# Kernel tuning notes

Measured on AMD Instinct MI355X. Metric: run time of the kernel, lower is better.

## Reference

```python
import jax, jax.numpy as jnp
import numpy as np

N, E, DIM, H, EDIM = 50000, 800000, 128, 4, 16
C = DIM // H  # per-head channels = 32

def _ln(x, g, b, eps=1e-5):
    mu = jnp.mean(x, -1, keepdims=True)
    var = jnp.mean((x - mu) ** 2, -1, keepdims=True)
    return (x - mu) * jax.lax.rsqrt(var + eps) * g + b

def setup_inputs() -> dict:
    key = jax.random.key(0)
    ks = jax.random.split(key, 16)
    s = lambda d: 1.0 / np.sqrt(d)
    inp = {
        'x': jax.random.normal(ks[0], (N, DIM), jnp.float32),
        'edge_index_s': jax.random.randint(ks[1], (2, E), 0, N, jnp.int64),
        'edge_attr_s': jax.random.normal(ks[2], (E, EDIM), jnp.float32),
        'Wq': jax.random.normal(ks[3], (DIM, DIM), jnp.float32) * s(DIM),
        'bq': jnp.zeros((DIM,), jnp.float32),
        'Wk': jax.random.normal(ks[4], (DIM, DIM), jnp.float32) * s(DIM),
        'bk': jnp.zeros((DIM,), jnp.float32),
        'Wv': jax.random.normal(ks[5], (DIM, DIM), jnp.float32) * s(DIM),
        'bv': jnp.zeros((DIM,), jnp.float32),
        'We': jax.random.normal(ks[6], (EDIM, DIM), jnp.float32) * s(EDIM),
        'be': jnp.zeros((DIM,), jnp.float32),
        'Ws': jax.random.normal(ks[7], (DIM, DIM), jnp.float32) * s(DIM),
        'bs': jnp.zeros((DIM,), jnp.float32),
        'Wbeta': jax.random.normal(ks[8], (3 * DIM, 1), jnp.float32) * s(3 * DIM),
        'g1': jnp.ones((DIM,), jnp.float32),
        'b1': jnp.zeros((DIM,), jnp.float32),
        'Wf1': jax.random.normal(ks[9], (DIM, 4 * DIM), jnp.float32) * s(DIM),
        'bf1': jnp.zeros((4 * DIM,), jnp.float32),
        'Wf2': jax.random.normal(ks[10], (4 * DIM, DIM), jnp.float32) * s(4 * DIM),
        'bf2': jnp.zeros((DIM,), jnp.float32),
        'g2': jnp.ones((DIM,), jnp.float32),
        'b2': jnp.zeros((DIM,), jnp.float32),
    }
    return inp

def reference(x, edge_index_s, edge_attr_s, Wq, bq, Wk, bk, Wv, bv, We, be,
              Ws, bs, Wbeta, g1, b1, Wf1, bf1, Wf2, bf2, g2, b2):
    src, dst = edge_index_s[0], edge_index_s[1]
    # project + reshape to [N, H, C]
    q = (x @ Wq + bq).reshape(N, H, C)
    k = (x @ Wk + bk).reshape(N, H, C)
    v = (x @ Wv + bv).reshape(N, H, C)
    e = (edge_attr_s @ We + be).reshape(E, H, C)
    # gather along edges (irregular access)
    kj = k[src] + e  # [E, H, C]
    vj = v[src] + e
    alpha = jnp.einsum('ehc,ehc->eh', q[dst], kj) / jnp.sqrt(jnp.float32(C))
    # segment softmax over incoming edges of each dst node
    m = jax.ops.segment_max(alpha, dst, num_segments=N)  # [N, H]
    a = jnp.exp(alpha - m[dst])
    denom = jax.ops.segment_sum(a, dst, num_segments=N)
    a = a / (denom[dst] + 1e-16)
    out = jax.ops.segment_sum(a[:, :, None] * vj, dst, num_segments=N)  # [N, H, C]
    out = out.reshape(N, DIM)
    # beta-gated skip (TransformerConv beta=True)
    xr = x @ Ws + bs
    beta = jax.nn.sigmoid(jnp.concatenate([out, xr, out - xr], -1) @ Wbeta)  # [N, 1]
    xs = beta * xr + (1.0 - beta) * out
    # residual + LN + FFN + LN
    h = _ln(x + xs, g1, b1)
    ff = jax.nn.relu(h @ Wf1 + bf1) @ Wf2 + bf2
    return _ln(h + ff, g2, b2)
```

## Files before the change

kernel.cpp:

```cpp
#include <hip/hip_runtime.h>
#include <hip/hip_bf16.h>

#define NN 50000
#define EE 800000
#define DIMM 128

typedef __attribute__((ext_vector_type(8))) short bf16x8;
typedef __attribute__((ext_vector_type(8))) unsigned short us8;
typedef __attribute__((ext_vector_type(4))) float f32x4;

static __device__ __forceinline__ unsigned short f2bf(float f) {
    unsigned int u = __float_as_uint(f);
    unsigned int r = (u + 0x7fffu + ((u >> 16) & 1u)) >> 16;
    return (unsigned short)r;
}
static __device__ __forceinline__ float bf2f(unsigned short s) {
    return __uint_as_float(((unsigned int)s) << 16);
}

__global__ __launch_bounds__(256) void pack_w(
    const float* __restrict__ Wq, const float* __restrict__ Wk,
    const float* __restrict__ Wv, const float* __restrict__ Ws,
    const float* __restrict__ bq, const float* __restrict__ bk,
    const float* __restrict__ bv, const float* __restrict__ bs,
    const float* __restrict__ Wf1, const float* __restrict__ Wf2,
    unsigned short* __restrict__ wqkvsT, unsigned short* __restrict__ wf1T,
    unsigned short* __restrict__ wf2T, float* __restrict__ biasq)
{
    int i = blockIdx.x * 256 + threadIdx.x;
    if (i < 65536) {
        int n = i >> 7, k = i & 127;
        int sel = n >> 7, col = n & 127;
        const float* W = sel == 0 ? Wq : sel == 1 ? Wk : sel == 2 ? Wv : Ws;
        wqkvsT[i] = f2bf(W[k * 128 + col]);
    } else if (i < 131072) {
        int j = i - 65536; int n = j >> 7, k = j & 127;
        wf1T[j] = f2bf(Wf1[k * 512 + n]);
    } else if (i < 196608) {
        int j = i - 131072; int n = j >> 9, k = j & 511;
        wf2T[j] = f2bf(Wf2[k * 128 + n]);
    } else if (i < 197120) {
        int j = i - 196608; int sel = j >> 7;
        const float* bp = sel == 0 ? bq : sel == 1 ? bk : sel == 2 ? bv : bs;
        biasq[j] = bp[j & 127];
    }
}

template<bool A_BF16, int EPI>
__global__ __launch_bounds__(256) void gemm_k(
    const void* __restrict__ Ap, const unsigned short* __restrict__ Bt,
    const float* __restrict__ bias, void* __restrict__ Cp,
    float* __restrict__ qb, unsigned short* __restrict__ kvb, float* __restrict__ xrb,
    int M, int Nn, int K)
{
    __shared__ unsigned short As[128][72];
    __shared__ unsigned short Bs[128][72];
    int tid = threadIdx.x;
    int nb = Nn >> 7;
    int bm = blockIdx.x / nb, bn = blockIdx.x % nb;
    int w = tid >> 6, lane = tid & 63;
    int wm = w >> 1, wn = w & 1;
    int lr = lane & 15, quad = lane >> 4;

    f32x4 acc[4][4];
    #pragma unroll
    for (int i = 0; i < 4; i++)
        #pragma unroll
        for (int j = 0; j < 4; j++) { f32x4 z = {0.f, 0.f, 0.f, 0.f}; acc[i][j] = z; }

    for (int kc = 0; kc < K; kc += 64) {
        #pragma unroll
        for (int it = 0; it < 4; ++it) {
            int row = it * 32 + (tid >> 3);
            int k8 = (tid & 7) * 8;
            int rg = bm * 128 + row;
            us8 st = {0, 0, 0, 0, 0, 0, 0, 0};
            if (rg < M) {
                if constexpr (A_BF16) {
                    st = *(const us8*)((const unsigned short*)Ap + (size_t)rg * K + kc + k8);
                } else {
                    const float* src = (const float*)Ap + (size_t)rg * K + kc + k8;
                    float4 f0 = *(const float4*)src;
                    float4 f1 = *(const float4*)(src + 4);
                    st[0] = f2bf(f0.x); st[1] = f2bf(f0.y); st[2] = f2bf(f0.z); st[3] = f2bf(f0.w);
                    st[4] = f2bf(f1.x); st[5] = f2bf(f1.y); st[6] = f2bf(f1.z); st[7] = f2bf(f1.w);
                }
            }
            *(us8*)&As[row][k8] = st;
            *(us8*)&Bs[row][k8] = *(const us8*)(Bt + (size_t)(bn * 128 + row) * K + kc + k8);
        }
        __syncthreads();
        #pragma unroll
        for (int kk = 0; kk < 2; ++kk) {
            bf16x8 af[4], bfr[4];
            #pragma unroll
            for (int mi = 0; mi < 4; mi++)
                af[mi] = *(const bf16x8*)&As[wm * 64 + mi * 16 + lr][kk * 32 + quad * 8];
            #pragma unroll
            for (int ni = 0; ni < 4; ni++)
                bfr[ni] = *(const bf16x8*)&Bs[wn * 64 + ni * 16 + lr][kk * 32 + quad * 8];
            #pragma unroll
            for (int mi = 0; mi < 4; mi++)
                #pragma unroll
                for (int ni = 0; ni < 4; ni++)
                    acc[mi][ni] = __builtin_amdgcn_mfma_f32_16x16x32_bf16(af[mi], bfr[ni], acc[mi][ni], 0, 0, 0);
        }
        __syncthreads();
    }
    #pragma unroll
    for (int mi = 0; mi < 4; mi++) {
        #pragma unroll
        for (int ni = 0; ni < 4; ni++) {
            int cg = bn * 128 + wn * 64 + ni * 16 + lr;
            float bv = bias[cg];
            #pragma unroll
            for (int r = 0; r < 4; r++) {
                int rg = bm * 128 + wm * 64 + mi * 16 + quad * 4 + r;
                if (rg < M) {
                    float val = acc[mi][ni][r] + bv;
                    if constexpr (EPI == 0) {
                        ((float*)Cp)[(size_t)rg * Nn + cg] = val;
                    } else if constexpr (EPI == 1) {
                        val = fmaxf(val, 0.f);
                        ((unsigned short*)Cp)[(size_t)rg * Nn + cg] = f2bf(val);
                    } else {
                        int sel = cg >> 7, c = cg & 127;
                        if (sel == 0)      qb[(size_t)rg * 128 + c] = val;
                        else if (sel == 1) kvb[(size_t)rg * 256 + 2 * c] = f2bf(val);
                        else if (sel == 2) kvb[(size_t)rg * 256 + 2 * c + 1] = f2bf(val);
                        else               xrb[(size_t)rg * 128 + c] = val;
                    }
                }
            }
        }
    }
}

__global__ __launch_bounds__(256) void hist_k(const int* __restrict__ dst, int* __restrict__ deg) {
    int e = blockIdx.x * 256 + threadIdx.x;
    if (e < EE) atomicAdd(&deg[dst[e]], 1);
}

__global__ __launch_bounds__(256) void scan_phaseA(const int* __restrict__ deg, int* __restrict__ rs,
                                                   int* __restrict__ bsum) {
    __shared__ int sm[256];
    int tid = threadIdx.x;
    int i = blockIdx.x * 256 + tid;
    int v = (i < NN) ? deg[i] : 0;
    sm[tid] = v;
    __syncthreads();
    #pragma unroll
    for (int off = 1; off < 256; off <<= 1) {
        int t = 0;
        if (tid >= off) t = sm[tid - off];
        __syncthreads();
        if (tid >= off) sm[tid] += t;
        __syncthreads();
    }
    if (i < NN) rs[i] = sm[tid] - v;
    if (tid == 255) bsum[blockIdx.x] = sm[255];
}

__global__ __launch_bounds__(256) void scan_phaseB(int* __restrict__ bsum, int nb) {
    __shared__ int sm[256];
    int tid = threadIdx.x;
    int v = (tid < nb) ? bsum[tid] : 0;
    sm[tid] = v;
    __syncthreads();
    #pragma unroll
    for (int off = 1; off < 256; off <<= 1) {
        int t = 0;
        if (tid >= off) t = sm[tid - off];
        __syncthreads();
        if (tid >= off) sm[tid] += t;
        __syncthreads();
    }
    if (tid < nb) bsum[tid] = sm[tid] - v;
}

__global__ __launch_bounds__(256) void scan_phaseC(int* __restrict__ rs, const int* __restrict__ bsum) {
    int i = blockIdx.x * 256 + threadIdx.x;
    if (i < NN) rs[i] += bsum[blockIdx.x];
    if (i == 0) rs[NN] = EE;
}

__global__ __launch_bounds__(256) void scatter_k(
    const int* __restrict__ src, const int* __restrict__ dst,
    const float* __restrict__ eattr, const int* __restrict__ rs,
    int* __restrict__ cur, int* __restrict__ srcs_sorted,
    unsigned short* __restrict__ eas)
{
    int e = blockIdx.x * 256 + threadIdx.x;
    if (e < EE) {
        int d = dst[e];
        int p = atomicAdd(&cur[d], 1);
        int pos = rs[d] + p;
        srcs_sorted[pos] = src[e];
        const float* ap = eattr + (size_t)e * 16;
        float4 a0 = *(const float4*)ap;
        float4 a1 = *(const float4*)(ap + 4);
        float4 a2 = *(const float4*)(ap + 8);
        float4 a3 = *(const float4*)(ap + 12);
        us8 lo, hi;
        lo[0] = f2bf(a0.x); lo[1] = f2bf(a0.y); lo[2] = f2bf(a0.z); lo[3] = f2bf(a0.w);
        lo[4] = f2bf(a1.x); lo[5] = f2bf(a1.y); lo[6] = f2bf(a1.z); lo[7] = f2bf(a1.w);
        hi[0] = f2bf(a2.x); hi[1] = f2bf(a2.y); hi[2] = f2bf(a2.z); hi[3] = f2bf(a2.w);
        hi[4] = f2bf(a3.x); hi[5] = f2bf(a3.y); hi[6] = f2bf(a3.z); hi[7] = f2bf(a3.w);
        *(us8*)(eas + (size_t)pos * 16)     = lo;
        *(us8*)(eas + (size_t)pos * 16 + 8) = hi;
    }
}

__global__ __launch_bounds__(256, 3) void attn_kernel(
    const float* __restrict__ q, const unsigned int* __restrict__ kvb,
    const float* __restrict__ xr, const float* __restrict__ x,
    const unsigned short* __restrict__ eas, const int* __restrict__ srcs,
    const int* __restrict__ rs,
    const float* __restrict__ We, const float* __restrict__ be,
    const float* __restrict__ Wbeta,
    const float* __restrict__ gamma1, const float* __restrict__ beta1,
    float* __restrict__ hout, unsigned int* __restrict__ hbf)
{
    int wave = threadIdx.x >> 6;
    int lane = threadIdx.x & 63;
    int n = blockIdx.x * 4 + wave;
    if (n >= NN) return;
    int c0 = lane * 2, c1 = c0 + 1;
    int jlane = lane & 15;
    int hbase = lane & 48;

    float be0 = be[c0], be1 = be[c1];

    float2 q2 = *(const float2*)(q + (size_t)n * 128 + c0);
    q2.x *= 0.17677669529663687f;
    q2.y *= 0.17677669529663687f;

    float qbe = q2.x * be0 + q2.y * be1;
    qbe += __shfl_xor(qbe, 1); qbe += __shfl_xor(qbe, 2);
    qbe += __shfl_xor(qbe, 4); qbe += __shfl_xor(qbe, 8);
    float qwe = 0.f;
    #pragma unroll
    for (int j = 0; j < 16; j++) {
        float u = q2.x * We[j * 128 + c0] + q2.y * We[j * 128 + c1];
        u += __shfl_xor(u, 1); u += __shfl_xor(u, 2);
        u += __shfl_xor(u, 4); u += __shfl_xor(u, 8);
        if (jlane == j) qwe = u;
    }

    float l = 0.f, a0 = 0.f, a1 = 0.f, s = 0.f;
    int beg = rs[n], end = rs[n + 1];

    int sr0[8], sr1[8];
    unsigned short ea0[8], ea1[8];
    uint2 kv0[8], kv1[8];

#define LOADMETA(g, SR, EA) { \
    _Pragma("unroll") \
    for (int j = 0; j < 8; j++) { \
        int idx = min((g) + j, EE - 1); \
        SR[j] = srcs[idx]; \
        EA[j] = eas[(size_t)idx * 16 + jlane]; \
    } }
#define GATHER(SR, KV) { \
    _Pragma("unroll") \
    for (int j = 0; j < 8; j++) \
        KV[j] = *(const uint2*)(kvb + (size_t)SR[j] * 128 + (lane << 1)); }
#define COMPUTE(g, EA, KV) { \
    int cnt = end - (g); \
    _Pragma("unroll") \
    for (int j = 0; j < 8; j++) { \
        if (j < cnt) { \
            float ea = bf2f(EA[j]); \
            unsigned int kx = KV[j].x, ky = KV[j].y; \
            float k0 = __uint_as_float(kx << 16); \
            float v0 = __uint_as_float(kx & 0xffff0000u); \
            float k1 = __uint_as_float(ky << 16); \
            float v1 = __uint_as_float(ky & 0xffff0000u); \
            float part = fmaf(q2.x, k0, fmaf(q2.y, k1, qwe * ea)); \
            part += __shfl_xor(part, 1); \
            part += __shfl_xor(part, 2); \
            part += __shfl_xor(part, 4); \
            part += __shfl_xor(part, 8); \
            float wgt = __expf(part + qbe); \
            l += wgt; \
            a0 = fmaf(wgt, v0, a0); \
            a1 = fmaf(wgt, v1, a1); \
            s = fmaf(wgt, ea, s); \
        } } }

    LOADMETA(beg, sr0, ea0)
    GATHER(sr0, kv0)
    LOADMETA(beg + 8, sr1, ea1)
    for (int g = beg; g < end; g += 16) {
        GATHER(sr1, kv1)
        COMPUTE(g, ea0, kv0)
        LOADMETA(g + 16, sr0, ea0)
        GATHER(sr0, kv0)
        COMPUTE(g + 8, ea1, kv1)
        LOADMETA(g + 24, sr1, ea1)
    }
#undef LOADMETA
#undef GATHER
#undef COMPUTE

    float eo0 = l * be0, eo1 = l * be1;
    #pragma unroll
    for (int j = 0; j < 16; j++) {
        float sj = __shfl(s, hbase + j);
        eo0 = fmaf(sj, We[j * 128 + c0], eo0);
        eo1 = fmaf(sj, We[j * 128 + c1], eo1);
    }
    a0 += eo0; a1 += eo1;

    float inv = l > 0.f ? 1.f / l : 0.f;
    float o0 = a0 * inv, o1 = a1 * inv;

    float wbo0 = Wbeta[c0],        wbo1 = Wbeta[c1];
    float wbx0 = Wbeta[128 + c0],  wbx1 = Wbeta[128 + c1];
    float wbd0 = Wbeta[256 + c0],  wbd1 = Wbeta[256 + c1];
    float2 xr2 = *(const float2*)(xr + (size_t)n * 128 + c0);
    float bl = o0 * wbo0 + o1 * wbo1 + xr2.x * wbx0 + xr2.y * wbx1
             + (o0 - xr2.x) * wbd0 + (o1 - xr2.y) * wbd1;
    #pragma unroll
    for (int off = 1; off < 64; off <<= 1) bl += __shfl_xor(bl, off);
    float beta = 1.f / (1.f + __expf(-bl));
    float xs0 = beta * xr2.x + (1.f - beta) * o0;
    float xs1 = beta * xr2.y + (1.f - beta) * o1;

    float2 xv = *(const float2*)(x + (size_t)n * 128 + c0);
    float t0 = xv.x + xs0, t1 = xv.y + xs1;
    float sm = t0 + t1;
    #pragma unroll
    for (int off = 1; off < 64; off <<= 1) sm += __shfl_xor(sm, off);
    float mu = sm * (1.f / 128.f);
    float d0 = t0 - mu, d1 = t1 - mu;
    float vv = d0 * d0 + d1 * d1;
    #pragma unroll
    for (int off = 1; off < 64; off <<= 1) vv += __shfl_xor(vv, off);
    float is = rsqrtf(vv * (1.f / 128.f) + 1e-5f);
    float h0 = d0 * is * gamma1[c0] + beta1[c0];
    float h1 = d1 * is * gamma1[c1] + beta1[c1];
    *(float2*)(hout + (size_t)n * 128 + c0) = make_float2(h0, h1);
    hbf[(size_t)n * 64 + lane] = (unsigned int)f2bf(h0) | ((unsigned int)f2bf(h1) << 16);
}

__global__ __launch_bounds__(256) void ln2_k(
    const float* __restrict__ h, const float* __restrict__ ff2,
    const float* __restrict__ gamma2, const float* __restrict__ beta2,
    float* __restrict__ out)
{
    int wave = threadIdx.x >> 6;
    int lane = threadIdx.x & 63;
    int n = blockIdx.x * 4 + wave;
    if (n >= NN) return;
    int c0 = lane * 2;
    float2 hv = *(const float2*)(h + (size_t)n * 128 + c0);
    float2 fv = *(const float2*)(ff2 + (size_t)n * 128 + c0);
    float t0 = hv.x + fv.x, t1 = hv.y + fv.y;
    float sm = t0 + t1;
    #pragma unroll
    for (int off = 1; off < 64; off <<= 1) sm += __shfl_xor(sm, off);
    float mu = sm * (1.f / 128.f);
    float d0 = t0 - mu, d1 = t1 - mu;
    float vv = d0 * d0 + d1 * d1;
    #pragma unroll
    for (int off = 1; off < 64; off <<= 1) vv += __shfl_xor(vv, off);
    float is = rsqrtf(vv * (1.f / 128.f) + 1e-5f);
    float o0 = d0 * is * gamma2[c0] + beta2[c0];
    float o1 = d1 * is * gamma2[c0 + 1] + beta2[c0 + 1];
    *(float2*)(out + (size_t)n * 128 + c0) = make_float2(o0, o1);
}

extern "C" void kernel_launch(void* const* d_in, const int* in_sizes, int n_in,
                              void* d_out, int out_size, void* d_ws, size_t ws_size,
                              hipStream_t stream) {
    const float* x      = (const float*)d_in[0];
    const int*   eindex = (const int*)d_in[1];
    const float* eattr  = (const float*)d_in[2];
    const float* Wq = (const float*)d_in[3];  const float* bq = (const float*)d_in[4];
    const float* Wk = (const float*)d_in[5];  const float* bk = (const float*)d_in[6];
    const float* Wv = (const float*)d_in[7];  const float* bv = (const float*)d_in[8];
    const float* We = (const float*)d_in[9];  const float* be = (const float*)d_in[10];
    const float* Ws = (const float*)d_in[11]; const float* bs = (const float*)d_in[12];
    const float* Wbeta = (const float*)d_in[13];
    const float* g1 = (const float*)d_in[14]; const float* b1 = (const float*)d_in[15];
    const float* Wf1 = (const float*)d_in[16]; const float* bf1 = (const float*)d_in[17];
    const float* Wf2 = (const float*)d_in[18]; const float* bf2 = (const float*)d_in[19];
    const float* g2 = (const float*)d_in[20]; const float* b2 = (const float*)d_in[21];

    char* ws = (char*)d_ws;
    size_t off = 0;
    #define ALLOC(ptr, type, bytes) type* ptr = (type*)(ws + off); off = (off + (size_t)(bytes) + 255) & ~(size_t)255;
    ALLOC(wqkvsT, unsigned short, 512 * 128 * 2)
    ALLOC(wf1T,   unsigned short, 512 * 128 * 2)
    ALLOC(wf2T,   unsigned short, 128 * 512 * 2)
    ALLOC(biasq,  float,          512 * 4)
    ALLOC(qb,     float,          (size_t)NN * 128 * 4)
    ALLOC(kvb,    unsigned short, (size_t)NN * 256 * 2)
    ALLOC(xrb,    float,          (size_t)NN * 128 * 4)
    ALLOC(h,      float,          (size_t)NN * 128 * 4)
    ALLOC(hbf,    unsigned int,   (size_t)NN * 128 * 2)
    ALLOC(deg,    int,            2 * NN * 4)
    ALLOC(row_start, int,         (NN + 1) * 4)
    ALLOC(bsum,   int,            1024)
    ALLOC(srcs_sorted, int,       (size_t)EE * 4)
    ALLOC(eas,    unsigned short, (size_t)EE * 16 * 2)
    #undef ALLOC
    int* cursor = deg + NN;
    unsigned short* ff1 = (unsigned short*)qb;
    float* ff2 = xrb;

    hipMemsetAsync(deg, 0, (size_t)2 * NN * 4, stream);

    pack_w<<<770, 256, 0, stream>>>(Wq, Wk, Wv, Ws, bq, bk, bv, bs, Wf1, Wf2,
                                    wqkvsT, wf1T, wf2T, biasq);

    gemm_k<false, 2><<<391 * 4, 256, 0, stream>>>(x, wqkvsT, biasq, nullptr,
                                                  qb, kvb, xrb, NN, 512, 128);

    hist_k<<<3125, 256, 0, stream>>>(eindex + EE, deg);
    scan_phaseA<<<196, 256, 0, stream>>>(deg, row_start, bsum);
    scan_phaseB<<<1, 256, 0, stream>>>(bsum, 196);
    scan_phaseC<<<196, 256, 0, stream>>>(row_start, bsum);
    scatter_k<<<3125, 256, 0, stream>>>(eindex, eindex + EE, eattr, row_start,
                                        cursor, srcs_sorted, eas);

    attn_kernel<<<12500, 256, 0, stream>>>(qb, (const unsigned int*)kvb, xrb, x,
                                           eas, srcs_sorted, row_start,
                                           We, be, Wbeta, g1, b1, h, hbf);

    gemm_k<true, 1><<<391 * 4, 256, 0, stream>>>(hbf, wf1T, bf1, ff1,
                                                 nullptr, nullptr, nullptr, NN, 512, 128);
    gemm_k<true, 0><<<391 * 1, 256, 0, stream>>>(ff1, wf2T, bf2, ff2,
                                                 nullptr, nullptr, nullptr, NN, 128, 512);

    ln2_k<<<12500, 256, 0, stream>>>(h, ff2, g2, b2, (float*)d_out);
}
```

Measured before the change: 531.7 us.

## Precompute q·We in separate kernel, use DPP reductions, tighten attention pipeline

Moves the per-node q·We projection out of the attention kernel into a new qwe_k kernel that writes a small per-node buffer, which the attention kernel now just loads. The 16-lane shuffle reductions are replaced with DPP row-shift adds, the edge loop's prefetch is restructured to skip out-of-range loads and exit early, and the occupancy hint is raised from 3 to 4 waves. The goal is less per-edge reduction latency and fewer registers in the attention kernel. In exchange it adds an extra launch and a round trip through a buffer of about 12.8 MB.

```diff
diff --git a/kernel.cpp b/kernel.cpp
--- a/kernel.cpp
+++ b/kernel.cpp
@@ -17,6 +17,13 @@
 static __device__ __forceinline__ float bf2f(unsigned short s) {
     return __uint_as_float(((unsigned int)s) << 16);
 }
+
+#define RED16(v) do { int _t; \
+    _t = __builtin_amdgcn_update_dpp(0, __float_as_int(v), 0x128, 0xF, 0xF, true); v += __int_as_float(_t); \
+    _t = __builtin_amdgcn_update_dpp(0, __float_as_int(v), 0x124, 0xF, 0xF, true); v += __int_as_float(_t); \
+    _t = __builtin_amdgcn_update_dpp(0, __float_as_int(v), 0x122, 0xF, 0xF, true); v += __int_as_float(_t); \
+    _t = __builtin_amdgcn_update_dpp(0, __float_as_int(v), 0x121, 0xF, 0xF, true); v += __int_as_float(_t); \
+} while (0)
 
 __global__ __launch_bounds__(256) void pack_w(
     const float* __restrict__ Wq, const float* __restrict__ Wk,
@@ -136,6 +143,26 @@
     }
 }
 
+__global__ __launch_bounds__(256) void qwe_k(
+    const float* __restrict__ q, const float* __restrict__ We,
+    float* __restrict__ qweb)
+{
+    int wave = threadIdx.x >> 6, lane = threadIdx.x & 63;
+    int n = blockIdx.x * 4 + wave;
+    if (n >= NN) return;
+    int head = lane >> 4, j = lane & 15;
+    const float* qp = q + (size_t)n * 128 + head * 32;
+    const float* wp = We + j * 128 + head * 32;
+    float acc = 0.f;
+    #pragma unroll
+    for (int c = 0; c < 32; c += 4) {
+        float4 qv = *(const float4*)(qp + c);
+        float4 wv = *(const float4*)(wp + c);
+        acc += qv.x * wv.x + qv.y * wv.y + qv.z * wv.z + qv.w * wv.w;
+    }
+    qweb[(size_t)n * 64 + lane] = acc * 0.17677669529663687f;
+}
+
 __global__ __launch_bounds__(256) void hist_k(const int* __restrict__ dst, int* __restrict__ deg) {
     int e = blockIdx.x * 256 + threadIdx.x;
     if (e < EE) atomicAdd(&deg[dst[e]], 1);
@@ -211,11 +238,11 @@
     }
 }
 
-__global__ __launch_bounds__(256, 3) void attn_kernel(
+__global__ __launch_bounds__(256, 4) void attn_kernel(
     const float* __restrict__ q, const unsigned int* __restrict__ kvb,
     const float* __restrict__ xr, const float* __restrict__ x,
     const unsigned short* __restrict__ eas, const int* __restrict__ srcs,
-    const int* __restrict__ rs,
+    const int* __restrict__ rs, const float* __restrict__ qweb,
     const float* __restrict__ We, const float* __restrict__ be,
     const float* __restrict__ Wbeta,
     const float* __restrict__ gamma1, const float* __restrict__ beta1,
@@ -236,16 +263,8 @@
     q2.y *= 0.17677669529663687f;
 
     float qbe = q2.x * be0 + q2.y * be1;
-    qbe += __shfl_xor(qbe, 1); qbe += __shfl_xor(qbe, 2);
-    qbe += __shfl_xor(qbe, 4); qbe += __shfl_xor(qbe, 8);
-    float qwe = 0.f;
-    #pragma unroll
-    for (int j = 0; j < 16; j++) {
-        float u = q2.x * We[j * 128 + c0] + q2.y * We[j * 128 + c1];
-        u += __shfl_xor(u, 1); u += __shfl_xor(u, 2);
-        u += __shfl_xor(u, 4); u += __shfl_xor(u, 8);
-        if (jlane == j) qwe = u;
-    }
+    RED16(qbe);
+    float qwe = qweb[(size_t)n * 64 + lane];
 
     float l = 0.f, a0 = 0.f, a1 = 0.f, s = 0.f;
     int beg = rs[n], end = rs[n + 1];
@@ -277,10 +296,7 @@
             float k1 = __uint_as_float(ky << 16); \
             float v1 = __uint_as_float(ky & 0xffff0000u); \
             float part = fmaf(q2.x, k0, fmaf(q2.y, k1, qwe * ea)); \
-            part += __shfl_xor(part, 1); \
-            part += __shfl_xor(part, 2); \
-            part += __shfl_xor(part, 4); \
-            part += __shfl_xor(part, 8); \
+            RED16(part); \
             float wgt = __expf(part + qbe); \
             l += wgt; \
             a0 = fmaf(wgt, v0, a0); \
@@ -288,16 +304,19 @@
             s = fmaf(wgt, ea, s); \
         } } }
 
-    LOADMETA(beg, sr0, ea0)
-    GATHER(sr0, kv0)
-    LOADMETA(beg + 8, sr1, ea1)
-    for (int g = beg; g < end; g += 16) {
-        GATHER(sr1, kv1)
-        COMPUTE(g, ea0, kv0)
-        LOADMETA(g + 16, sr0, ea0)
+    if (beg < end) {
+        LOADMETA(beg, sr0, ea0)
         GATHER(sr0, kv0)
-        COMPUTE(g + 8, ea1, kv1)
-        LOADMETA(g + 24, sr1, ea1)
+        for (int g = beg; ; g += 16) {
+            bool m1 = (g + 8 < end);
+            if (m1) { LOADMETA(g + 8, sr1, ea1) GATHER(sr1, kv1) }
+            COMPUTE(g, ea0, kv0)
+            if (!m1) break;
+            bool m2 = (g + 16 < end);
+            if (m2) { LOADMETA(g + 16, sr0, ea0) GATHER(sr0, kv0) }
+            COMPUTE(g + 8, ea1, kv1)
+            if (!m2) break;
+        }
     }
 #undef LOADMETA
 #undef GATHER
@@ -400,6 +419,7 @@
     ALLOC(xrb,    float,          (size_t)NN * 128 * 4)
     ALLOC(h,      float,          (size_t)NN * 128 * 4)
     ALLOC(hbf,    unsigned int,   (size_t)NN * 128 * 2)
+    ALLOC(qweb,   float,          (size_t)NN * 64 * 4)
     ALLOC(deg,    int,            2 * NN * 4)
     ALLOC(row_start, int,         (NN + 1) * 4)
     ALLOC(bsum,   int,            1024)
@@ -418,6 +438,8 @@
     gemm_k<false, 2><<<391 * 4, 256, 0, stream>>>(x, wqkvsT, biasq, nullptr,
                                                   qb, kvb, xrb, NN, 512, 128);
 
+    qwe_k<<<12500, 256, 0, stream>>>(qb, We, qweb);
+
     hist_k<<<3125, 256, 0, stream>>>(eindex + EE, deg);
     scan_phaseA<<<196, 256, 0, stream>>>(deg, row_start, bsum);
     scan_phaseB<<<1, 256, 0, stream>>>(bsum, 196);
@@ -426,7 +448,7 @@
                                         cursor, srcs_sorted, eas);
 
     attn_kernel<<<12500, 256, 0, stream>>>(qb, (const unsigned int*)kvb, xrb, x,
-                                           eas, srcs_sorted, row_start,
+                                           eas, srcs_sorted, row_start, qweb,
                                            We, be, Wbeta, g1, b1, h, hbf);
 
     gemm_k<true, 1><<<391 * 4, 256, 0, stream>>>(hbf, wf1T, bf1, ff1,
```

Measured after the change: 523.9 us. Within noise of the previous version (-1.5%).
